# Optimization experiments

Measured on AMD Instinct MI355X. Metric: run time of the kernel, lower is better.

The kernel has to match this reference:

```python
import jax, jax.numpy as jnp
import numpy as np
from jax import lax

INPUT_SIZE = 3
HIDDEN = 32
SEQ = 24
BATCH = 131072
FC1 = 16


def setup_inputs() -> dict:
    key = jax.random.key(0)
    ks = jax.random.split(key, 9)
    s_ih = 1.0 / np.sqrt(HIDDEN)
    # PyTorch LSTM params: weight_ih (4H, input), weight_hh (4H, H), biases (4H,)
    return {
        "x": jax.random.normal(ks[0], (BATCH, SEQ, INPUT_SIZE), dtype=jnp.float32),
        "w_ih": jax.random.uniform(ks[1], (4 * HIDDEN, INPUT_SIZE), minval=-s_ih, maxval=s_ih, dtype=jnp.float32),
        "w_hh": jax.random.uniform(ks[2], (4 * HIDDEN, HIDDEN), minval=-s_ih, maxval=s_ih, dtype=jnp.float32),
        "b_ih": jax.random.uniform(ks[3], (4 * HIDDEN,), minval=-s_ih, maxval=s_ih, dtype=jnp.float32),
        "b_hh": jax.random.uniform(ks[4], (4 * HIDDEN,), minval=-s_ih, maxval=s_ih, dtype=jnp.float32),
        "w1": jax.random.uniform(ks[5], (FC1, HIDDEN), minval=-s_ih, maxval=s_ih, dtype=jnp.float32),
        "b1": jax.random.uniform(ks[6], (FC1,), minval=-s_ih, maxval=s_ih, dtype=jnp.float32),
        "w2": jax.random.uniform(ks[7], (1, FC1), minval=-0.25, maxval=0.25, dtype=jnp.float32),
        "b2": jax.random.uniform(ks[8], (1,), minval=-0.25, maxval=0.25, dtype=jnp.float32),
    }


def reference(x, w_ih, w_hh, b_ih, b_hh, w1, b1, w2, b2):
    B = x.shape[0]
    b = b_ih + b_hh  # fuse the two bias vectors

    def step(carry, xt):
        h, c = carry
        # gates: (B, 4H) in PyTorch order [i, f, g, o]
        gates = xt @ w_ih.T + h @ w_hh.T + b
        i, f, g, o = jnp.split(gates, 4, axis=-1)
        c_new = jax.nn.sigmoid(f) * c + jax.nn.sigmoid(i) * jnp.tanh(g)
        h_new = jax.nn.sigmoid(o) * jnp.tanh(c_new)
        return (h_new, c_new), None

    h0 = jnp.zeros((B, HIDDEN), dtype=x.dtype)
    c0 = jnp.zeros((B, HIDDEN), dtype=x.dtype)
    xs = jnp.transpose(x, (1, 0, 2))  # (T, B, F)
    (h_last, _), _ = lax.scan(step, (h0, c0), xs)

    # Head: Linear(H,16) -> ReLU -> Dropout(identity in eval) -> Linear(16,1)
    hid = jax.nn.relu(h_last @ w1.T + b1)
    logit = hid @ w2.T + b2  # (B, 1)
    return logit
```

## Files before the change

### kernel.cpp

```cpp
#include <hip/hip_runtime.h>


typedef short bf16x8 __attribute__((ext_vector_type(8)));
typedef short bf16x4 __attribute__((ext_vector_type(4)));
typedef float f32x4 __attribute__((ext_vector_type(4)));
typedef float f32x2 __attribute__((ext_vector_type(2)));

#define L2E 1.4426950408889634f

#if __has_builtin(__builtin_amdgcn_mfma_f32_16x16x16bf16_1k)
#define HAVE_MFMA16 1
#else
#define HAVE_MFMA16 0
#endif

__device__ __forceinline__ unsigned f2bf(float f) {
    unsigned u = __float_as_uint(f);
    return (u + 0x7FFFu + ((u >> 16) & 1u)) >> 16;
}
__device__ __forceinline__ float fexp2(float v) { return __builtin_amdgcn_exp2f(v); }
__device__ __forceinline__ float frcp(float v)  { return __builtin_amdgcn_rcpf(v); }
__device__ __forceinline__ unsigned cvtpk(float lo, float hi) {
    unsigned r;
    asm("v_cvt_pk_bf16_f32 %0, %1, %2" : "=v"(r) : "v"(lo), "v"(hi));
    return r;
}

__device__ __forceinline__ unsigned act2(f32x2 vi, f32x2 vf, f32x2 vg, f32x2 vo,
                                         f32x2& cc)
{
    f32x2 ex, ey, ef, ew, ez, r1, r2;
    ex[0] = fexp2(-vi[0]); ex[1] = fexp2(-vi[1]);
    ey[0] = fexp2(vg[0]);  ey[1] = fexp2(vg[1]);
    ef[0] = fexp2(-vf[0]); ef[1] = fexp2(-vf[1]);
    const f32x2 one = {1.f, 1.f};
    f32x2 axy = (one + ex) * (one + ey);
    f32x2 efp = one + ef;
    f32x2 dd  = axy * efp;
    r1[0] = frcp(dd[0]); r1[1] = frcp(dd[1]);
    const f32x2 K2 = {2.f * L2E, 2.f * L2E};
    f32x2 igs = (ey * K2 - K2) * efp * r1;
    f32x2 fs  = axy * r1;
    cc = fs * cc + igs;
    ew[0] = fexp2(-vo[0]); ew[1] = fexp2(-vo[1]);
    ez[0] = fexp2(cc[0]);  ez[1] = fexp2(cc[1]);
    f32x2 d2 = (one + ew) * (one + ez);
    r2[0] = frcp(d2[0]); r2[1] = frcp(d2[1]);
    f32x2 hn = (ez - one) * r2;
    return cvtpk(hn[0], hn[1]);
}

__global__ __launch_bounds__(256, 4)
void lstm_fused(const float* __restrict__ x,
                const float* __restrict__ w_ih,
                const float* __restrict__ w_hh,
                const float* __restrict__ b_ih,
                const float* __restrict__ b_hh,
                const float* __restrict__ w1,
                const float* __restrict__ b1,
                const float* __restrict__ w2,
                const float* __restrict__ b2,
                float* __restrict__ out)
{
    __shared__ int2  xq[24 * 64];
    __shared__ float w1s[512];
    __shared__ float b1s[16];
    __shared__ float w2s[16];
    __shared__ float b2s;

    const int tid  = threadIdx.x;
    const int lane = tid & 63;
    const int wv   = tid >> 6;
    const int c    = lane & 15;
    const int g    = lane >> 4;
    const int blockBase = blockIdx.x * 64;

    for (int i = tid; i < 512; i += 256) w1s[i] = w1[i];
    if (tid < 16) { b1s[tid] = b1[tid]; w2s[tid] = w2[tid]; }
    if (tid == 16) b2s = b2[0];

    for (int it = 0; it < 6; ++it) {
        int p = tid + it * 256;
        int n = p / 24;
        int t = p - n * 24;
        const float* xp = x + ((blockBase + n) * 24 + t) * 3;
        unsigned lo = f2bf(xp[0]) | (f2bf(xp[1]) << 16);
        unsigned hi = f2bf(xp[2]) | (0x3F80u << 16);
        xq[t * 64 + n] = make_int2((int)lo, (int)hi);
    }

    bf16x8 whh[8];
#if HAVE_MFMA16
    bf16x4 wib[8];
#else
    bf16x8 wib[8];
#endif
    const int ubase = 8 * (c >> 2) + (c & 3);
#pragma unroll
    for (int G = 0; G < 4; ++G) {
        const float scale = (G == 2) ? (2.f * L2E) : L2E;
#pragma unroll
        for (int p = 0; p < 2; ++p) {
            const int row = G * 32 + ubase + 4 * p;
            const float* wr = w_hh + row * 32 + g * 8;
            bf16x8 a;
#pragma unroll
            for (int e = 0; e < 8; ++e) a[e] = (short)f2bf(wr[e] * scale);
            whh[G * 2 + p] = a;
            short c0 = 0, c1 = 0, c2 = 0, c3 = 0;
            if (g == 0) {
                c0 = (short)f2bf(w_ih[row * 3 + 0] * scale);
                c1 = (short)f2bf(w_ih[row * 3 + 1] * scale);
                c2 = (short)f2bf(w_ih[row * 3 + 2] * scale);
                c3 = (short)f2bf((b_ih[row] + b_hh[row]) * scale);
            }
#if HAVE_MFMA16
            bf16x4 bb = {c0, c1, c2, c3};
#else
            bf16x8 bb = {c0, c1, c2, c3, 0, 0, 0, 0};
#endif
            wib[G * 2 + p] = bb;
        }
    }

    __syncthreads();

    f32x2 cz = {0.f, 0.f};
    f32x2 cst2[4] = {cz, cz, cz, cz};

    union { unsigned u[4]; bf16x8 v; } hreg;
    hreg.u[0] = hreg.u[1] = hreg.u[2] = hreg.u[3] = 0u;

    const int xidx = wv * 16 + c;
    int2 xv = xq[xidx];

#pragma unroll 1
    for (int t = 0; t < 24; ++t) {
        const int tn = (t < 23) ? t + 1 : 23;
        int2 xnxt = xq[tn * 64 + xidx];

        bf16x8 hf = hreg.v;
        int xlo = (g == 0) ? xv.x : 0;
        int xhi = (g == 0) ? xv.y : 0;
#if HAVE_MFMA16
        union { int2 i2; bf16x4 v; } xu;
        xu.i2 = make_int2(xlo, xhi);
        bf16x4 xf = xu.v;
#else
        union { int4 i4; bf16x8 v; } xu;
        xu.i4 = make_int4(xlo, xhi, 0, 0);
        bf16x8 xf = xu.v;
#endif

#pragma unroll
        for (int p = 0; p < 2; ++p) {
            f32x4 z = {0.f, 0.f, 0.f, 0.f};
            f32x4 ai = z, af = z, ag = z, ao = z;
            ai = __builtin_amdgcn_mfma_f32_16x16x32_bf16(whh[0 + p], hf, ai, 0, 0, 0);
            af = __builtin_amdgcn_mfma_f32_16x16x32_bf16(whh[2 + p], hf, af, 0, 0, 0);
            ag = __builtin_amdgcn_mfma_f32_16x16x32_bf16(whh[4 + p], hf, ag, 0, 0, 0);
            ao = __builtin_amdgcn_mfma_f32_16x16x32_bf16(whh[6 + p], hf, ao, 0, 0, 0);
#if HAVE_MFMA16
            ai = __builtin_amdgcn_mfma_f32_16x16x16bf16_1k(wib[0 + p], xf, ai, 0, 0, 0);
            af = __builtin_amdgcn_mfma_f32_16x16x16bf16_1k(wib[2 + p], xf, af, 0, 0, 0);
            ag = __builtin_amdgcn_mfma_f32_16x16x16bf16_1k(wib[4 + p], xf, ag, 0, 0, 0);
            ao = __builtin_amdgcn_mfma_f32_16x16x16bf16_1k(wib[6 + p], xf, ao, 0, 0, 0);
#else
            ai = __builtin_amdgcn_mfma_f32_16x16x32_bf16(wib[0 + p], xf, ai, 0, 0, 0);
            af = __builtin_amdgcn_mfma_f32_16x16x32_bf16(wib[2 + p], xf, af, 0, 0, 0);
            ag = __builtin_amdgcn_mfma_f32_16x16x32_bf16(wib[4 + p], xf, ag, 0, 0, 0);
            ao = __builtin_amdgcn_mfma_f32_16x16x32_bf16(wib[6 + p], xf, ao, 0, 0, 0);
#endif
            f32x2 vi0 = {ai[0], ai[1]}, vi1 = {ai[2], ai[3]};
            f32x2 vf0 = {af[0], af[1]}, vf1 = {af[2], af[3]};
            f32x2 vg0 = {ag[0], ag[1]}, vg1 = {ag[2], ag[3]};
            f32x2 vo0 = {ao[0], ao[1]}, vo1 = {ao[2], ao[3]};
            hreg.u[2 * p + 0] = act2(vi0, vf0, vg0, vo0, cst2[2 * p + 0]);
            hreg.u[2 * p + 1] = act2(vi1, vf1, vg1, vo1, cst2[2 * p + 1]);
        }
        xv = xnxt;
    }

    float hfin[8];
#pragma unroll
    for (int d = 0; d < 4; ++d) {
        hfin[2 * d + 0] = __uint_as_float(hreg.u[d] << 16);
        hfin[2 * d + 1] = __uint_as_float(hreg.u[d] & 0xFFFF0000u);
    }
    float hid[16];
#pragma unroll
    for (int q = 0; q < 16; ++q) {
        const float4* wrow = (const float4*)(w1s + q * 32 + g * 8);
        float4 wa = wrow[0], wb = wrow[1];
        float s = wa.x * hfin[0] + wa.y * hfin[1] + wa.z * hfin[2] + wa.w * hfin[3]
                + wb.x * hfin[4] + wb.y * hfin[5] + wb.z * hfin[6] + wb.w * hfin[7];
        s += __shfl_xor(s, 16);
        s += __shfl_xor(s, 32);
        hid[q] = s;
    }
    float po = b2s;
#pragma unroll
    for (int q = 0; q < 16; ++q)
        po = fmaf(fmaxf(hid[q] + b1s[q], 0.f), w2s[q], po);
    if (g == 0) out[blockBase + xidx] = po;
}

extern "C" void kernel_launch(void* const* d_in, const int* in_sizes, int n_in,
                              void* d_out, int out_size, void* d_ws, size_t ws_size,
                              hipStream_t stream) {
    (void)in_sizes; (void)n_in; (void)d_ws; (void)ws_size; (void)out_size;
    const float* x    = (const float*)d_in[0];
    const float* w_ih = (const float*)d_in[1];
    const float* w_hh = (const float*)d_in[2];
    const float* b_ih = (const float*)d_in[3];
    const float* b_hh = (const float*)d_in[4];
    const float* w1   = (const float*)d_in[5];
    const float* b1   = (const float*)d_in[6];
    const float* w2   = (const float*)d_in[7];
    const float* b2   = (const float*)d_in[8];
    float* outp = (float*)d_out;

    dim3 grid(131072 / 64);
    dim3 block(256);
    hipLaunchKernelGGL(lstm_fused, grid, block, 0, stream,
                       x, w_ih, w_hh, b_ih, b_hh, w1, b1, w2, b2, outp);
}
```

Measured before the change: 105.8 us.

## Switch MFMA to fp16 and interleave two independent sequence tiles per wave

```diff
diff --git a/kernel.cpp b/kernel.cpp
--- a/kernel.cpp
+++ b/kernel.cpp
@@ -1,33 +1,25 @@
 #include <hip/hip_runtime.h>
 
 
-typedef short bf16x8 __attribute__((ext_vector_type(8)));
-typedef short bf16x4 __attribute__((ext_vector_type(4)));
+typedef _Float16 f16x8 __attribute__((ext_vector_type(8)));
+typedef _Float16 f16x4 __attribute__((ext_vector_type(4)));
+typedef _Float16 f16x2 __attribute__((ext_vector_type(2)));
 typedef float f32x4 __attribute__((ext_vector_type(4)));
 typedef float f32x2 __attribute__((ext_vector_type(2)));
 
 #define L2E 1.4426950408889634f
 
-#if __has_builtin(__builtin_amdgcn_mfma_f32_16x16x16bf16_1k)
+#if __has_builtin(__builtin_amdgcn_mfma_f32_16x16x16f16)
 #define HAVE_MFMA16 1
 #else
 #define HAVE_MFMA16 0
 #endif
 
-__device__ __forceinline__ unsigned f2bf(float f) {
-    unsigned u = __float_as_uint(f);
-    return (u + 0x7FFFu + ((u >> 16) & 1u)) >> 16;
-}
 __device__ __forceinline__ float fexp2(float v) { return __builtin_amdgcn_exp2f(v); }
 __device__ __forceinline__ float frcp(float v)  { return __builtin_amdgcn_rcpf(v); }
-__device__ __forceinline__ unsigned cvtpk(float lo, float hi) {
-    unsigned r;
-    asm("v_cvt_pk_bf16_f32 %0, %1, %2" : "=v"(r) : "v"(lo), "v"(hi));
-    return r;
-}
-
-__device__ __forceinline__ unsigned act2(f32x2 vi, f32x2 vf, f32x2 vg, f32x2 vo,
-                                         f32x2& cc)
+
+__device__ __forceinline__ f16x2 act2(f32x2 vi, f32x2 vf, f32x2 vg, f32x2 vo,
+                                      f32x2& cc)
 {
     f32x2 ex, ey, ef, ew, ez, r1, r2;
     ex[0] = fexp2(-vi[0]); ex[1] = fexp2(-vi[1]);
@@ -47,10 +39,11 @@
     f32x2 d2 = (one + ew) * (one + ez);
     r2[0] = frcp(d2[0]); r2[1] = frcp(d2[1]);
     f32x2 hn = (ez - one) * r2;
-    return cvtpk(hn[0], hn[1]);
+    f16x2 r; r[0] = (_Float16)hn[0]; r[1] = (_Float16)hn[1];
+    return r;
 }
 
-__global__ __launch_bounds__(256, 4)
+__global__ __launch_bounds__(256, 3)
 void lstm_fused(const float* __restrict__ x,
                 const float* __restrict__ w_ih,
                 const float* __restrict__ w_hh,
@@ -62,7 +55,7 @@
                 const float* __restrict__ b2,
                 float* __restrict__ out)
 {
-    __shared__ int2  xq[24 * 64];
+    __shared__ int2  xq[24 * 128];
     __shared__ float w1s[512];
     __shared__ float b1s[16];
     __shared__ float w2s[16];
@@ -73,27 +66,30 @@
     const int wv   = tid >> 6;
     const int c    = lane & 15;
     const int g    = lane >> 4;
-    const int blockBase = blockIdx.x * 64;
+    const int blockBase = blockIdx.x * 128;
 
     for (int i = tid; i < 512; i += 256) w1s[i] = w1[i];
     if (tid < 16) { b1s[tid] = b1[tid]; w2s[tid] = w2[tid]; }
     if (tid == 16) b2s = b2[0];
 
-    for (int it = 0; it < 6; ++it) {
+    for (int it = 0; it < 12; ++it) {
         int p = tid + it * 256;
         int n = p / 24;
         int t = p - n * 24;
         const float* xp = x + ((blockBase + n) * 24 + t) * 3;
-        unsigned lo = f2bf(xp[0]) | (f2bf(xp[1]) << 16);
-        unsigned hi = f2bf(xp[2]) | (0x3F80u << 16);
-        xq[t * 64 + n] = make_int2((int)lo, (int)hi);
-    }
-
-    bf16x8 whh[8];
-#if HAVE_MFMA16
-    bf16x4 wib[8];
-#else
-    bf16x8 wib[8];
+        union { f16x4 h; int2 i2; } tq;
+        tq.h[0] = (_Float16)xp[0];
+        tq.h[1] = (_Float16)xp[1];
+        tq.h[2] = (_Float16)xp[2];
+        tq.h[3] = (_Float16)1.0f;
+        xq[t * 128 + n] = tq.i2;
+    }
+
+    f16x8 whh[8];
+#if HAVE_MFMA16
+    f16x4 wib[8];
+#else
+    f16x8 wib[8];
 #endif
     const int ubase = 8 * (c >> 2) + (c & 3);
 #pragma unroll
@@ -103,21 +99,21 @@
         for (int p = 0; p < 2; ++p) {
             const int row = G * 32 + ubase + 4 * p;
             const float* wr = w_hh + row * 32 + g * 8;
-            bf16x8 a;
-#pragma unroll
-            for (int e = 0; e < 8; ++e) a[e] = (short)f2bf(wr[e] * scale);
+            f16x8 a;
+#pragma unroll
+            for (int e = 0; e < 8; ++e) a[e] = (_Float16)(wr[e] * scale);
             whh[G * 2 + p] = a;
-            short c0 = 0, c1 = 0, c2 = 0, c3 = 0;
+            _Float16 c0 = 0, c1 = 0, c2 = 0, c3 = 0;
             if (g == 0) {
-                c0 = (short)f2bf(w_ih[row * 3 + 0] * scale);
-                c1 = (short)f2bf(w_ih[row * 3 + 1] * scale);
-                c2 = (short)f2bf(w_ih[row * 3 + 2] * scale);
-                c3 = (short)f2bf((b_ih[row] + b_hh[row]) * scale);
+                c0 = (_Float16)(w_ih[row * 3 + 0] * scale);
+                c1 = (_Float16)(w_ih[row * 3 + 1] * scale);
+                c2 = (_Float16)(w_ih[row * 3 + 2] * scale);
+                c3 = (_Float16)((b_ih[row] + b_hh[row]) * scale);
             }
 #if HAVE_MFMA16
-            bf16x4 bb = {c0, c1, c2, c3};
-#else
-            bf16x8 bb = {c0, c1, c2, c3, 0, 0, 0, 0};
+            f16x4 bb = {c0, c1, c2, c3};
+#else
+            f16x8 bb = {c0, c1, c2, c3, 0, 0, 0, 0};
 #endif
             wib[G * 2 + p] = bb;
         }
@@ -126,83 +122,90 @@
     __syncthreads();
 
     f32x2 cz = {0.f, 0.f};
-    f32x2 cst2[4] = {cz, cz, cz, cz};
-
-    union { unsigned u[4]; bf16x8 v; } hreg;
-    hreg.u[0] = hreg.u[1] = hreg.u[2] = hreg.u[3] = 0u;
-
-    const int xidx = wv * 16 + c;
-    int2 xv = xq[xidx];
+    f32x2 cst2[2][4] = {{cz, cz, cz, cz}, {cz, cz, cz, cz}};
+    union hu_t { f16x2 p2[4]; f16x8 v; int4 i4; } hreg[2];
+#pragma unroll
+    for (int s = 0; s < 2; ++s) hreg[s].i4 = make_int4(0, 0, 0, 0);
+
+    const int n0 = wv * 16 + c;
+    int2 xv[2];
+    xv[0] = xq[n0];
+    xv[1] = xq[n0 + 64];
 
 #pragma unroll 1
     for (int t = 0; t < 24; ++t) {
         const int tn = (t < 23) ? t + 1 : 23;
-        int2 xnxt = xq[tn * 64 + xidx];
-
-        bf16x8 hf = hreg.v;
-        int xlo = (g == 0) ? xv.x : 0;
-        int xhi = (g == 0) ? xv.y : 0;
-#if HAVE_MFMA16
-        union { int2 i2; bf16x4 v; } xu;
-        xu.i2 = make_int2(xlo, xhi);
-        bf16x4 xf = xu.v;
-#else
-        union { int4 i4; bf16x8 v; } xu;
-        xu.i4 = make_int4(xlo, xhi, 0, 0);
-        bf16x8 xf = xu.v;
-#endif
-
-#pragma unroll
-        for (int p = 0; p < 2; ++p) {
-            f32x4 z = {0.f, 0.f, 0.f, 0.f};
-            f32x4 ai = z, af = z, ag = z, ao = z;
-            ai = __builtin_amdgcn_mfma_f32_16x16x32_bf16(whh[0 + p], hf, ai, 0, 0, 0);
-            af = __builtin_amdgcn_mfma_f32_16x16x32_bf16(whh[2 + p], hf, af, 0, 0, 0);
-            ag = __builtin_amdgcn_mfma_f32_16x16x32_bf16(whh[4 + p], hf, ag, 0, 0, 0);
-            ao = __builtin_amdgcn_mfma_f32_16x16x32_bf16(whh[6 + p], hf, ao, 0, 0, 0);
-#if HAVE_MFMA16
-            ai = __builtin_amdgcn_mfma_f32_16x16x16bf16_1k(wib[0 + p], xf, ai, 0, 0, 0);
-            af = __builtin_amdgcn_mfma_f32_16x16x16bf16_1k(wib[2 + p], xf, af, 0, 0, 0);
-            ag = __builtin_amdgcn_mfma_f32_16x16x16bf16_1k(wib[4 + p], xf, ag, 0, 0, 0);
-            ao = __builtin_amdgcn_mfma_f32_16x16x16bf16_1k(wib[6 + p], xf, ao, 0, 0, 0);
-#else
-            ai = __builtin_amdgcn_mfma_f32_16x16x32_bf16(wib[0 + p], xf, ai, 0, 0, 0);
-            af = __builtin_amdgcn_mfma_f32_16x16x32_bf16(wib[2 + p], xf, af, 0, 0, 0);
-            ag = __builtin_amdgcn_mfma_f32_16x16x32_bf16(wib[4 + p], xf, ag, 0, 0, 0);
-            ao = __builtin_amdgcn_mfma_f32_16x16x32_bf16(wib[6 + p], xf, ao, 0, 0, 0);
-#endif
-            f32x2 vi0 = {ai[0], ai[1]}, vi1 = {ai[2], ai[3]};
-            f32x2 vf0 = {af[0], af[1]}, vf1 = {af[2], af[3]};
-            f32x2 vg0 = {ag[0], ag[1]}, vg1 = {ag[2], ag[3]};
-            f32x2 vo0 = {ao[0], ao[1]}, vo1 = {ao[2], ao[3]};
-            hreg.u[2 * p + 0] = act2(vi0, vf0, vg0, vo0, cst2[2 * p + 0]);
-            hreg.u[2 * p + 1] = act2(vi1, vf1, vg1, vo1, cst2[2 * p + 1]);
+        int2 xn0 = xq[tn * 128 + n0];
+        int2 xn1 = xq[tn * 128 + n0 + 64];
+
+#pragma unroll
+        for (int s = 0; s < 2; ++s) {
+            f16x8 hf = hreg[s].v;
+            int xlo = (g == 0) ? xv[s].x : 0;
+            int xhi = (g == 0) ? xv[s].y : 0;
+#if HAVE_MFMA16
+            union { int2 i2; f16x4 v; } xu;
+            xu.i2 = make_int2(xlo, xhi);
+            f16x4 xf = xu.v;
+#else
+            union { int4 i4; f16x8 v; } xu;
+            xu.i4 = make_int4(xlo, xhi, 0, 0);
+            f16x8 xf = xu.v;
+#endif
+
+#pragma unroll
+            for (int p = 0; p < 2; ++p) {
+                f32x4 z = {0.f, 0.f, 0.f, 0.f};
+                f32x4 ai = z, af = z, ag = z, ao = z;
+                ai = __builtin_amdgcn_mfma_f32_16x16x32_f16(whh[0 + p], hf, ai, 0, 0, 0);
+                af = __builtin_amdgcn_mfma_f32_16x16x32_f16(whh[2 + p], hf, af, 0, 0, 0);
+                ag = __builtin_amdgcn_mfma_f32_16x16x32_f16(whh[4 + p], hf, ag, 0, 0, 0);
+                ao = __builtin_amdgcn_mfma_f32_16x16x32_f16(whh[6 + p], hf, ao, 0, 0, 0);
+#if HAVE_MFMA16
+                ai = __builtin_amdgcn_mfma_f32_16x16x16f16(wib[0 + p], xf, ai, 0, 0, 0);
+                af = __builtin_amdgcn_mfma_f32_16x16x16f16(wib[2 + p], xf, af, 0, 0, 0);
+                ag = __builtin_amdgcn_mfma_f32_16x16x16f16(wib[4 + p], xf, ag, 0, 0, 0);
+                ao = __builtin_amdgcn_mfma_f32_16x16x16f16(wib[6 + p], xf, ao, 0, 0, 0);
+#else
+                ai = __builtin_amdgcn_mfma_f32_16x16x32_f16(wib[0 + p], xf, ai, 0, 0, 0);
+                af = __builtin_amdgcn_mfma_f32_16x16x32_f16(wib[2 + p], xf, af, 0, 0, 0);
+                ag = __builtin_amdgcn_mfma_f32_16x16x32_f16(wib[4 + p], xf, ag, 0, 0, 0);
+                ao = __builtin_amdgcn_mfma_f32_16x16x32_f16(wib[6 + p], xf, ao, 0, 0, 0);
+#endif
+                f32x2 vi0 = {ai[0], ai[1]}, vi1 = {ai[2], ai[3]};
+                f32x2 vf0 = {af[0], af[1]}, vf1 = {af[2], af[3]};
+                f32x2 vg0 = {ag[0], ag[1]}, vg1 = {ag[2], ag[3]};
+                f32x2 vo0 = {ao[0], ao[1]}, vo1 = {ao[2], ao[3]};
+                hreg[s].p2[2 * p + 0] = act2(vi0, vf0, vg0, vo0, cst2[s][2 * p + 0]);
+                hreg[s].p2[2 * p + 1] = act2(vi1, vf1, vg1, vo1, cst2[s][2 * p + 1]);
+            }
         }
-        xv = xnxt;
-    }
-
-    float hfin[8];
-#pragma unroll
-    for (int d = 0; d < 4; ++d) {
-        hfin[2 * d + 0] = __uint_as_float(hreg.u[d] << 16);
-        hfin[2 * d + 1] = __uint_as_float(hreg.u[d] & 0xFFFF0000u);
-    }
-    float hid[16];
-#pragma unroll
-    for (int q = 0; q < 16; ++q) {
-        const float4* wrow = (const float4*)(w1s + q * 32 + g * 8);
-        float4 wa = wrow[0], wb = wrow[1];
-        float s = wa.x * hfin[0] + wa.y * hfin[1] + wa.z * hfin[2] + wa.w * hfin[3]
-                + wb.x * hfin[4] + wb.y * hfin[5] + wb.z * hfin[6] + wb.w * hfin[7];
-        s += __shfl_xor(s, 16);
-        s += __shfl_xor(s, 32);
-        hid[q] = s;
-    }
-    float po = b2s;
-#pragma unroll
-    for (int q = 0; q < 16; ++q)
-        po = fmaf(fmaxf(hid[q] + b1s[q], 0.f), w2s[q], po);
-    if (g == 0) out[blockBase + xidx] = po;
+        xv[0] = xn0;
+        xv[1] = xn1;
+    }
+
+#pragma unroll
+    for (int s = 0; s < 2; ++s) {
+        float hfin[8];
+#pragma unroll
+        for (int d = 0; d < 8; ++d) hfin[d] = (float)hreg[s].v[d];
+        float hid[16];
+#pragma unroll
+        for (int q = 0; q < 16; ++q) {
+            const float4* wrow = (const float4*)(w1s + q * 32 + g * 8);
+            float4 wa = wrow[0], wb = wrow[1];
+            float sm = wa.x * hfin[0] + wa.y * hfin[1] + wa.z * hfin[2] + wa.w * hfin[3]
+                     + wb.x * hfin[4] + wb.y * hfin[5] + wb.z * hfin[6] + wb.w * hfin[7];
+            sm += __shfl_xor(sm, 16);
+            sm += __shfl_xor(sm, 32);
+            hid[q] = sm;
+        }
+        float po = b2s;
+#pragma unroll
+        for (int q = 0; q < 16; ++q)
+            po = fmaf(fmaxf(hid[q] + b1s[q], 0.f), w2s[q], po);
+        if (g == 0) out[blockBase + s * 64 + n0] = po;
+    }
 }
 
 extern "C" void kernel_launch(void* const* d_in, const int* in_sizes, int n_in,
@@ -220,7 +223,7 @@
     const float* b2   = (const float*)d_in[8];
     float* outp = (float*)d_out;
 
-    dim3 grid(131072 / 64);
+    dim3 grid(131072 / 128);
     dim3 block(256);
     hipLaunchKernelGGL(lstm_fused, grid, block, 0, stream,
                        x, w_ih, w_hh, b_ih, b_hh, w1, b1, w2, b2, outp);
```

Result: faster. 102.7 us (-3.0%).
